# Optimization experiments

Measured on AMD Instinct MI355X. Metric: run time of the kernel, lower is better.

Reference implementation:

```python
import jax, jax.numpy as jnp
import numpy as np

NEG_SLOPE = 0.2   # PyG GATConv default negative_slope
BN_EPS = 1e-5
N_NODES = 50000
N_EDGES = 600000
N_GRAPHS = 64


def _gat_conv(x, W, att_src, att_dst, bias, src, dst, heads, out_ch, concat):
    """PyG GATConv (eval mode, self-loops already appended to src/dst).
    x: [N, in], W: [in, heads*out_ch], att_*: [heads, out_ch], bias: [heads*out_ch] or [out_ch].
    """
    n = x.shape[0]
    h = (x @ W).reshape(n, heads, out_ch)                  # [N, H, C]
    a_s = jnp.sum(h * att_src[None], axis=-1)              # [N, H]
    a_d = jnp.sum(h * att_dst[None], axis=-1)              # [N, H]
    logit = jax.nn.leaky_relu(a_s[src] + a_d[dst], NEG_SLOPE)  # [E, H]
    # segment softmax over destination node (every node has a self-loop -> no empty segment)
    m = jax.ops.segment_max(logit, dst, num_segments=n)
    p = jnp.exp(logit - m[dst])
    denom = jax.ops.segment_sum(p, dst, num_segments=n)
    alpha = p / (denom[dst] + 1e-16)                       # [E, H]
    out = jax.ops.segment_sum(h[src] * alpha[:, :, None], dst, num_segments=n)  # [N, H, C]
    out = out.reshape(n, heads * out_ch) if concat else out.mean(axis=1)
    return out + bias


def _bn(x, gamma, beta):
    mu = x.mean(axis=0)
    var = x.var(axis=0)
    return (x - mu) * jax.lax.rsqrt(var + BN_EPS) * gamma + beta


def setup_inputs() -> dict:
    key = jax.random.key(0)
    ks = jax.random.split(key, 20)
    hidden = 64
    d1_in, d1_out, h1 = 5, hidden // 2, 4          # 5 -> 32x4 = 128
    d2_in, d2_out, h2 = hidden * 2, hidden // 2, 4  # 128 -> 32x4 = 128
    d3_in, d3_out, h3 = hidden * 2, hidden, 1       # 128 -> 64

    def glorot(k, shape):
        fan = shape[0] + shape[-1]
        return jax.random.normal(k, shape, dtype=jnp.float32) * np.sqrt(2.0 / fan)

    inp = {
        "x": jax.random.normal(ks[0], (N_NODES, d1_in), dtype=jnp.float32),
        "edge_index": jax.random.randint(ks[1], (2, N_EDGES), 0, N_NODES),
        "batch": jnp.sort(jax.random.randint(ks[2], (N_NODES,), 0, N_GRAPHS)),
        # conv1
        "W1": glorot(ks[3], (d1_in, h1 * d1_out)),
        "a1_src": glorot(ks[4], (h1, d1_out)),
        "a1_dst": glorot(ks[5], (h1, d1_out)),
        "b1": jnp.zeros((h1 * d1_out,), dtype=jnp.float32),
        "g1": jnp.ones((h1 * d1_out,), dtype=jnp.float32),
        "be1": jnp.zeros((h1 * d1_out,), dtype=jnp.float32),
        # conv2
        "W2": glorot(ks[6], (d2_in, h2 * d2_out)),
        "a2_src": glorot(ks[7], (h2, d2_out)),
        "a2_dst": glorot(ks[8], (h2, d2_out)),
        "b2": jnp.zeros((h2 * d2_out,), dtype=jnp.float32),
        "g2": jnp.ones((h2 * d2_out,), dtype=jnp.float32),
        "be2": jnp.zeros((h2 * d2_out,), dtype=jnp.float32),
        # conv3 (single head, concat=False)
        "W3": glorot(ks[9], (d3_in, h3 * d3_out)),
        "a3_src": glorot(ks[10], (h3, d3_out)),
        "a3_dst": glorot(ks[11], (h3, d3_out)),
        "b3": jnp.zeros((d3_out,), dtype=jnp.float32),
    }
    return inp


def reference(x, edge_index, batch, W1, a1_src, a1_dst, b1, g1, be1,
              W2, a2_src, a2_dst, b2, g2, be2, W3, a3_src, a3_dst, b3):
    n = x.shape[0]
    loops = jnp.arange(n)
    src = jnp.concatenate([edge_index[0], loops])  # PyG add_self_loops=True
    dst = jnp.concatenate([edge_index[1], loops])

    h = jax.nn.elu(_bn(_gat_conv(x, W1, a1_src, a1_dst, b1, src, dst, 4, 32, True), g1, be1))
    h = jax.nn.elu(_bn(_gat_conv(h, W2, a2_src, a2_dst, b2, src, dst, 4, 32, True), g2, be2))
    h = jax.nn.elu(_gat_conv(h, W3, a3_src, a3_dst, b3, src, dst, 1, 64, False))

    counts = jax.ops.segment_sum(jnp.ones((n,), h.dtype), batch, num_segments=N_GRAPHS)
    mean_pool = jax.ops.segment_sum(h, batch, num_segments=N_GRAPHS) / jnp.maximum(counts, 1.0)[:, None]
    max_pool = jax.ops.segment_max(h, batch, num_segments=N_GRAPHS)
    max_pool = jnp.where(counts[:, None] > 0, max_pool, 0.0)
    return jnp.concatenate([mean_pool, max_pool], axis=1)  # [G, 128]
```

## Files before the change

kernel.cpp:

```cpp
#include <hip/hip_runtime.h>
#include <math.h>

#define NEG_SLOPE 0.2f
#define BN_EPS 1e-5f

typedef __attribute__((ext_vector_type(8))) short short8;
typedef __attribute__((ext_vector_type(4))) float f32x4;

__device__ __forceinline__ float lrelu_f(float x){ return x > 0.f ? x : NEG_SLOPE * x; }
__device__ __forceinline__ float elu_f(float x){ return x > 0.f ? x : __expf(x) - 1.f; }

__device__ __forceinline__ unsigned short f2bf(float f){
    unsigned u = __float_as_uint(f);
    return (unsigned short)((u + 0x7fffu + ((u >> 16) & 1u)) >> 16);
}
__device__ __forceinline__ float bf_lo(unsigned v){ return __uint_as_float(v << 16); }
__device__ __forceinline__ float bf_hi(unsigned v){ return __uint_as_float(v & 0xffff0000u); }
__device__ __forceinline__ float bf2f(unsigned short b){ return __uint_as_float((unsigned)b << 16); }

__device__ __forceinline__ unsigned enc_f(float x){
    unsigned b = __float_as_uint(x);
    return (b & 0x80000000u) ? ~b : (b | 0x80000000u);
}
__device__ __forceinline__ float dec_f(unsigned u){
    return __uint_as_float((u & 0x80000000u) ? (u & 0x7FFFFFFFu) : ~u);
}

__global__ void k_prep(const int* __restrict__ ei, int E0, int N, int Bc, int Bg,
                       const int* __restrict__ batch, int G,
                       int* __restrict__ counts, int* __restrict__ gp,
                       const float* __restrict__ W1, const float* __restrict__ a1s,
                       const float* __restrict__ a1d,
                       const float* __restrict__ W2, const float* __restrict__ W3,
                       unsigned short* __restrict__ wt2, unsigned short* __restrict__ wt3,
                       float* __restrict__ u_s, float* __restrict__ u_d){
    int b = blockIdx.x, tid = threadIdx.x;
    if (b < Bc){
        int i = b * 256 + tid, tot = E0 + N;
        if (i < tot){
            int dst = (i < E0) ? ei[E0 + i] : (i - E0);
            atomicAdd(&counts[dst], 1);
        }
    } else if (b < Bc + Bg){
        int i = (b - Bc) * 256 + tid;
        if (i < N){
            int bb = batch[i];
            if (i == 0){ for (int g = 0; g <= bb; ++g) gp[g] = 0; }
            else { int pb = batch[i - 1]; for (int g = pb + 1; g <= bb; ++g) gp[g] = i; }
            if (i == N - 1){ for (int g = bb + 1; g <= G; ++g) gp[g] = N; }
        }
    } else if (b < Bc + Bg + 96){
        int i = (b - Bc - Bg) * 256 + tid;
        if (i < 128 * 128){
            int k = i / 128, c = i % 128;
            wt2[c * 128 + k] = f2bf(W2[i]);
        } else if (i < 128 * 128 + 128 * 64){
            int j = i - 128 * 128;
            int k = j / 64, c = j % 64;
            wt3[c * 128 + k] = f2bf(W3[j]);
        }
    } else {
        if (tid < 40){
            int t2 = tid % 20;
            int k = t2 / 4, hh = t2 % 4;
            const float* att = (tid < 20) ? a1s : a1d;
            float s = 0.f;
            for (int j = 0; j < 32; ++j) s += W1[k * 128 + hh * 32 + j] * att[hh * 32 + j];
            if (tid < 20) u_s[k * 4 + hh] = s; else u_d[k * 4 + hh] = s;
        }
    }
}

__global__ void k_scan_part(const int* __restrict__ counts, int n, int* __restrict__ part){
    __shared__ int sh[256];
    int tid = threadIdx.x;
    int i = blockIdx.x * 256 + tid;
    int v = (i < n) ? counts[i] : 0;
    sh[tid] = v;
    __syncthreads();
    for (int o = 128; o > 0; o >>= 1){
        if (tid < o) sh[tid] += sh[tid + o];
        __syncthreads();
    }
    if (tid == 0) part[blockIdx.x] = sh[0];
}

__global__ void k_scan_write(const int* __restrict__ counts, const int* __restrict__ part,
                             int n, int* __restrict__ row_ptr){
    __shared__ int sh[256], rsh[256];
    __shared__ int offs;
    int tid = threadIdx.x, bid = blockIdx.x;
    int po = 0;
    for (int j = tid; j < bid; j += 256) po += part[j];
    rsh[tid] = po;
    __syncthreads();
    for (int o = 128; o > 0; o >>= 1){
        if (tid < o) rsh[tid] += rsh[tid + o];
        __syncthreads();
    }
    if (tid == 0) offs = rsh[0];
    __syncthreads();
    int i = bid * 256 + tid;
    int v = (i < n) ? counts[i] : 0;
    sh[tid] = v;
    __syncthreads();
    for (int o = 1; o < 256; o <<= 1){
        int t = (tid >= o) ? sh[tid - o] : 0;
        __syncthreads();
        sh[tid] += t;
        __syncthreads();
    }
    if (i < n) row_ptr[i] = offs + sh[tid] - v;
    if (bid == gridDim.x - 1 && tid == 255) row_ptr[n] = offs + sh[255];
}

__global__ void k_scatter(const int* __restrict__ ei, int E0, int N,
                          const int* __restrict__ row_ptr, int* __restrict__ cursor,
                          int* __restrict__ csr_src){
    int i = blockIdx.x * blockDim.x + threadIdx.x;
    int tot = E0 + N;
    if (i >= tot) return;
    int src, dst;
    if (i < E0){ src = ei[i]; dst = ei[E0 + i]; } else { src = dst = i - E0; }
    int pos = atomicAdd(&cursor[dst], 1);
    csr_src[row_ptr[dst] + pos] = src;
}

__launch_bounds__(512)
__global__ void k_agg1(const float* __restrict__ X, const float* __restrict__ W1,
                       const float* __restrict__ u_s, const float* __restrict__ u_d,
                       const int* __restrict__ row_ptr, const int* __restrict__ csr_src,
                       const float* __restrict__ bias, float* __restrict__ out, int N){
    int wid = threadIdx.x >> 6, lane = threadIdx.x & 63;
    long n = (long)blockIdx.x * 8 + wid;
    if (n >= N) return;
    int hh = lane >> 4;
    int c0 = lane * 2;
    float2 wv[5]; float us[5], ud[5];
#pragma unroll
    for (int k = 0; k < 5; ++k){
        wv[k] = *(const float2*)&W1[k * 128 + c0];
        us[k] = u_s[k * 4 + hh];
        ud[k] = u_d[k * 4 + hh];
    }
    float xd[5];
#pragma unroll
    for (int k = 0; k < 5; ++k) xd[k] = X[n * 5 + k];
    float ad = xd[0]*ud[0] + xd[1]*ud[1] + xd[2]*ud[2] + xd[3]*ud[3] + xd[4]*ud[4];
    int beg = row_ptr[n], end = row_ptr[n + 1];
    float accx = 0.f, accy = 0.f, dn = 0.f;
    int e = beg;
    for (; e + 2 <= end; e += 2){
        int s0 = csr_src[e], s1 = csr_src[e + 1];
        float a0[5], a1[5];
#pragma unroll
        for (int k = 0; k < 5; ++k){ a0[k] = X[(long)s0 * 5 + k]; a1[k] = X[(long)s1 * 5 + k]; }
        float as0 = a0[0]*us[0] + a0[1]*us[1] + a0[2]*us[2] + a0[3]*us[3] + a0[4]*us[4];
        float as1 = a1[0]*us[0] + a1[1]*us[1] + a1[2]*us[2] + a1[3]*us[3] + a1[4]*us[4];
        float p0 = __expf(lrelu_f(as0 + ad));
        float p1 = __expf(lrelu_f(as1 + ad));
        float hx0 = a0[0]*wv[0].x + a0[1]*wv[1].x + a0[2]*wv[2].x + a0[3]*wv[3].x + a0[4]*wv[4].x;
        float hy0 = a0[0]*wv[0].y + a0[1]*wv[1].y + a0[2]*wv[2].y + a0[3]*wv[3].y + a0[4]*wv[4].y;
        float hx1 = a1[0]*wv[0].x + a1[1]*wv[1].x + a1[2]*wv[2].x + a1[3]*wv[3].x + a1[4]*wv[4].x;
        float hy1 = a1[0]*wv[0].y + a1[1]*wv[1].y + a1[2]*wv[2].y + a1[3]*wv[3].y + a1[4]*wv[4].y;
        dn += p0 + p1;
        accx += p0 * hx0 + p1 * hx1;
        accy += p0 * hy0 + p1 * hy1;
    }
    if (e < end){
        int s0 = csr_src[e];
        float a0[5];
#pragma unroll
        for (int k = 0; k < 5; ++k) a0[k] = X[(long)s0 * 5 + k];
        float as0 = a0[0]*us[0] + a0[1]*us[1] + a0[2]*us[2] + a0[3]*us[3] + a0[4]*us[4];
        float p0 = __expf(lrelu_f(as0 + ad));
        float hx0 = a0[0]*wv[0].x + a0[1]*wv[1].x + a0[2]*wv[2].x + a0[3]*wv[3].x + a0[4]*wv[4].x;
        float hy0 = a0[0]*wv[0].y + a0[1]*wv[1].y + a0[2]*wv[2].y + a0[3]*wv[3].y + a0[4]*wv[4].y;
        dn += p0; accx += p0 * hx0; accy += p0 * hy0;
    }
    float inv = 1.f / dn;
    float2 o; o.x = accx * inv + bias[c0]; o.y = accy * inv + bias[c0 + 1];
    *(float2*)&out[n * 128 + c0] = o;
}

template<int OUT, int H, bool BN>
__launch_bounds__(256)
__global__ void k_gemm_mfma(const float* __restrict__ X, const unsigned short* __restrict__ Wt,
                            const float* __restrict__ atts, const float* __restrict__ attd,
                            const float* __restrict__ coefs, const float* __restrict__ coefb,
                            unsigned short* __restrict__ h, float* __restrict__ as_,
                            float* __restrict__ ad_, int N){
    constexpr int TM  = 64;
    constexpr int NCT = OUT / 16;
    constexpr int CPH = NCT / H;
    __shared__ unsigned short Xl[TM * 128];
    __shared__ unsigned short Wl[OUT * 128];
    int tid = threadIdx.x;
    long base = (long)blockIdx.x * TM;

    for (int i = tid; i < OUT * 16; i += 256){
        int r = i >> 4, g = i & 15;
        uint4 v = *(const uint4*)&Wt[r * 128 + g * 8];
        int gs = g ^ (r & 7);
        *(uint4*)&Wl[r * 128 + gs * 8] = v;
    }
    for (int i = tid; i < TM * 16; i += 256){
        int r = i >> 4, g = i & 15;
        long node = base + r;
        uint4 o;
        if (node < N){
            const float* xp = &X[node * 128 + g * 8];
            float f[8];
            *(float4*)&f[0] = *(const float4*)xp;
            *(float4*)&f[4] = *(const float4*)(xp + 4);
#pragma unroll
            for (int j = 0; j < 8; ++j){
                float v = f[j];
                if (BN) v = elu_f(fmaf(v, coefs[g * 8 + j], coefb[g * 8 + j]));
                f[j] = v;
            }
            o.x = (unsigned)f2bf(f[0]) | ((unsigned)f2bf(f[1]) << 16);
            o.y = (unsigned)f2bf(f[2]) | ((unsigned)f2bf(f[3]) << 16);
            o.z = (unsigned)f2bf(f[4]) | ((unsigned)f2bf(f[5]) << 16);
            o.w = (unsigned)f2bf(f[6]) | ((unsigned)f2bf(f[7]) << 16);
        } else {
            o.x = o.y = o.z = o.w = 0u;
        }
        int gs = g ^ (r & 7);
        *(uint4*)&Xl[r * 128 + gs * 8] = o;
    }
    __syncthreads();

    int wid = tid >> 6;
    int lane = tid & 63;
    int lr = lane & 15, lk = lane >> 4;

    short8 afrag[4];
    int arow = wid * 16 + lr;
#pragma unroll
    for (int ks = 0; ks < 4; ++ks){
        int g = ks * 4 + lk;
        int gs = g ^ (arow & 7);
        afrag[ks] = *(const short8*)&Xl[arow * 128 + gs * 8];
    }
    f32x4 acc[NCT];
#pragma unroll
    for (int ct = 0; ct < NCT; ++ct) acc[ct] = (f32x4){0.f, 0.f, 0.f, 0.f};
#pragma unroll
    for (int ct = 0; ct < NCT; ++ct){
        int brow = ct * 16 + lr;
#pragma unroll
        for (int ks = 0; ks < 4; ++ks){
            int g = ks * 4 + lk;
            int gs = g ^ (brow & 7);
            short8 bfrag = *(const short8*)&Wl[brow * 128 + gs * 8];
            acc[ct] = __builtin_amdgcn_mfma_f32_16x16x32_bf16(afrag[ks], bfrag, acc[ct], 0, 0, 0);
        }
    }
    float ps[H][4], pd[H][4];
#pragma unroll
    for (int hh = 0; hh < H; ++hh)
#pragma unroll
        for (int j = 0; j < 4; ++j){ ps[hh][j] = 0.f; pd[hh][j] = 0.f; }
#pragma unroll
    for (int ct = 0; ct < NCT; ++ct){
        int col = ct * 16 + lr;
        int hh = ct / CPH;
        float asv = atts[col], adv = attd[col];
#pragma unroll
        for (int j = 0; j < 4; ++j){
            float v = acc[ct][j];
            long node = base + wid * 16 + lk * 4 + j;
            if (node < N) h[node * OUT + col] = f2bf(v);
            ps[hh][j] += v * asv;
            pd[hh][j] += v * adv;
        }
    }
#pragma unroll
    for (int m = 1; m < 16; m <<= 1){
#pragma unroll
        for (int hh = 0; hh < H; ++hh)
#pragma unroll
            for (int j = 0; j < 4; ++j){
                ps[hh][j] += __shfl_xor(ps[hh][j], m);
                pd[hh][j] += __shfl_xor(pd[hh][j], m);
            }
    }
    if (lr == 0){
#pragma unroll
        for (int j = 0; j < 4; ++j){
            long node = base + wid * 16 + lk * 4 + j;
            if (node < N){
#pragma unroll
                for (int hh = 0; hh < H; ++hh){
                    as_[node * H + hh] = ps[hh][j];
                    ad_[node * H + hh] = pd[hh][j];
                }
            }
        }
    }
}

template<int C, int H, int ACT>
__global__ void k_agg(const unsigned short* __restrict__ h, const float* __restrict__ as_,
                      const float* __restrict__ ad_, const int* __restrict__ row_ptr,
                      const int* __restrict__ csr_src, const float* __restrict__ bias,
                      float* __restrict__ out, int N){
    constexpr int CPL = C / 64;
    constexpr int GROUP = C / H;
    int n = blockIdx.x;
    if (n >= N) return;
    int lane = threadIdx.x;
    int hh = (CPL * lane) / GROUP;
    float ad = ad_[n * H + hh];
    int beg = row_ptr[n], end = row_ptr[n + 1];
    float accx = 0.f, accy = 0.f, dn = 0.f;
    const unsigned* h32 = (const unsigned*)h;
    int e = beg;
    for (; e + 2 <= end; e += 2){
        int s0 = csr_src[e], s1 = csr_src[e + 1];
        float a0 = as_[s0 * H + hh], a1 = as_[s1 * H + hh];
        unsigned v0, v1; unsigned short w0, w1;
        if (CPL == 2){ v0 = h32[(long)s0 * 64 + lane]; v1 = h32[(long)s1 * 64 + lane]; }
        else { w0 = h[(long)s0 * 64 + lane]; w1 = h[(long)s1 * 64 + lane]; }
        float p0 = __expf(lrelu_f(a0 + ad));
        float p1 = __expf(lrelu_f(a1 + ad));
        dn += p0 + p1;
        if (CPL == 2){
            accx += p0 * bf_lo(v0) + p1 * bf_lo(v1);
            accy += p0 * bf_hi(v0) + p1 * bf_hi(v1);
        } else {
            accx += p0 * bf2f(w0) + p1 * bf2f(w1);
        }
    }
    if (e < end){
        int s0 = csr_src[e];
        float p0 = __expf(lrelu_f(as_[s0 * H + hh] + ad));
        dn += p0;
        if (CPL == 2){
            unsigned v0 = h32[(long)s0 * 64 + lane];
            accx += p0 * bf_lo(v0); accy += p0 * bf_hi(v0);
        } else {
            accx += p0 * bf2f(h[(long)s0 * 64 + lane]);
        }
    }
    float inv = 1.f / dn;
    if (CPL == 2){
        float vx = accx * inv + bias[2 * lane];
        float vy = accy * inv + bias[2 * lane + 1];
        if (ACT == 1){ vx = elu_f(vx); vy = elu_f(vy); }
        float2 o; o.x = vx; o.y = vy;
        *(float2*)&out[(long)n * C + 2 * lane] = o;
    } else {
        float v = accx * inv + bias[lane];
        if (ACT == 1) v = elu_f(v);
        out[(long)n * C + lane] = v;
    }
}

__launch_bounds__(256)
__global__ void k_bn_part(const float* __restrict__ x, int N,
                          float* __restrict__ ps, float* __restrict__ pq){
    __shared__ float4 lsum[256], lsq[256];
    int tid = threadIdx.x;
    int cq = tid & 31;
    int rg = tid >> 5;
    int rpb = (N + gridDim.x - 1) / gridDim.x;
    int lo = blockIdx.x * rpb;
    int hi = lo + rpb; if (hi > N) hi = N;
    float4 s = {0.f, 0.f, 0.f, 0.f}, q = {0.f, 0.f, 0.f, 0.f};
    int r = lo + rg;
    for (; r + 24 < hi; r += 32){
        float4 v0 = *(const float4*)&x[(long)r * 128 + cq * 4];
        float4 v1 = *(const float4*)&x[(long)(r + 8) * 128 + cq * 4];
        float4 v2 = *(const float4*)&x[(long)(r + 16) * 128 + cq * 4];
        float4 v3 = *(const float4*)&x[(long)(r + 24) * 128 + cq * 4];
        s.x += v0.x + v1.x + v2.x + v3.x;
        s.y += v0.y + v1.y + v2.y + v3.y;
        s.z += v0.z + v1.z + v2.z + v3.z;
        s.w += v0.w + v1.w + v2.w + v3.w;
        q.x += v0.x * v0.x + v1.x * v1.x + v2.x * v2.x + v3.x * v3.x;
        q.y += v0.y * v0.y + v1.y * v1.y + v2.y * v2.y + v3.y * v3.y;
        q.z += v0.z * v0.z + v1.z * v1.z + v2.z * v2.z + v3.z * v3.z;
        q.w += v0.w * v0.w + v1.w * v1.w + v2.w * v2.w + v3.w * v3.w;
    }
    for (; r < hi; r += 8){
        float4 v = *(const float4*)&x[(long)r * 128 + cq * 4];
        s.x += v.x; s.y += v.y; s.z += v.z; s.w += v.w;
        q.x += v.x * v.x; q.y += v.y * v.y; q.z += v.z * v.z; q.w += v.w * v.w;
    }
    lsum[tid] = s; lsq[tid] = q;
    __syncthreads();
    for (int o = 4; o > 0; o >>= 1){
        if (rg < o){
            float4 s2 = lsum[tid + o * 32], q2 = lsq[tid + o * 32];
            s.x += s2.x; s.y += s2.y; s.z += s2.z; s.w += s2.w;
            q.x += q2.x; q.y += q2.y; q.z += q2.z; q.w += q2.w;
            lsum[tid] = s; lsq[tid] = q;
        }
        __syncthreads();
    }
    if (rg == 0){
        *(float4*)&ps[(long)blockIdx.x * 128 + cq * 4] = s;
        *(float4*)&pq[(long)blockIdx.x * 128 + cq * 4] = q;
    }
}

__launch_bounds__(1024)
__global__ void k_bn_fin(const float* __restrict__ ps, const float* __restrict__ pq, int PB,
                         const float* __restrict__ g, const float* __restrict__ be,
                         float invN, float* __restrict__ cs, float* __restrict__ cb){
    __shared__ float sh_s[1024], sh_q[1024];
    int tid = threadIdx.x;
    int c = tid & 127, sl = tid >> 7;
    float s = 0.f, q = 0.f;
    for (int b = sl; b < PB; b += 8){
        s += ps[(long)b * 128 + c];
        q += pq[(long)b * 128 + c];
    }
    sh_s[tid] = s; sh_q[tid] = q;
    __syncthreads();
    for (int o = 4; o > 0; o >>= 1){
        if (sl < o){
            s += sh_s[tid + o * 128]; q += sh_q[tid + o * 128];
            sh_s[tid] = s; sh_q[tid] = q;
        }
        __syncthreads();
    }
    if (sl == 0){
        float mu = s * invN;
        float var = q * invN - mu * mu;
        float sc = g[c] * rsqrtf(var + BN_EPS);
        cs[c] = sc;
        cb[c] = be[c] - mu * sc;
    }
}

__global__ void k_pool_part(const float* __restrict__ x, const int* __restrict__ gp,
                            float* __restrict__ psum, unsigned* __restrict__ pmax){
    constexpr int S = 16;
    __shared__ float ssum[256], smax[256];
    int g = blockIdx.y;
    int split = blockIdx.x;
    int tid = threadIdx.x;
    int c = tid & 63, sub = tid >> 6;
    int beg = gp[g], end = gp[g + 1];
    int len = end - beg;
    int chunk = (len + S - 1) / S;
    int lo = beg + split * chunk;
    int hi = lo + chunk; if (hi > end) hi = end;
    if (lo >= hi) return;
    float s = 0.f, mx = -1e30f;
    for (int i = lo + sub; i < hi; i += 4){
        float v = x[(long)i * 64 + c];
        s += v; mx = fmaxf(mx, v);
    }
    ssum[tid] = s; smax[tid] = mx;
    __syncthreads();
    if (tid < 64){
        for (int k = 1; k < 4; ++k){ s += ssum[tid + 64 * k]; mx = fmaxf(mx, smax[tid + 64 * k]); }
        atomicAdd(&psum[g * 64 + c], s);
        atomicMax(&pmax[g * 64 + c], enc_f(mx));
    }
}

__global__ void k_pool_fin(const float* __restrict__ psum, const unsigned* __restrict__ pmax,
                           const int* __restrict__ gp, float* __restrict__ out){
    int g = blockIdx.x;
    int c = threadIdx.x;
    int cnt = gp[g + 1] - gp[g];
    float mean = (cnt > 0) ? psum[g * 64 + c] / (float)cnt : 0.f;
    float mx   = (cnt > 0) ? dec_f(pmax[g * 64 + c]) : 0.f;
    out[g * 128 + c]      = mean;
    out[g * 128 + 64 + c] = mx;
}

extern "C" void kernel_launch(void* const* d_in, const int* in_sizes, int n_in,
                              void* d_out, int out_size, void* d_ws, size_t ws_size,
                              hipStream_t stream){
    const float* x   = (const float*)d_in[0];
    const int*   ei  = (const int*)d_in[1];
    const int*   bat = (const int*)d_in[2];
    const float* W1  = (const float*)d_in[3];
    const float* a1s = (const float*)d_in[4];
    const float* a1d = (const float*)d_in[5];
    const float* b1  = (const float*)d_in[6];
    const float* g1  = (const float*)d_in[7];
    const float* be1 = (const float*)d_in[8];
    const float* W2  = (const float*)d_in[9];
    const float* a2s = (const float*)d_in[10];
    const float* a2d = (const float*)d_in[11];
    const float* b2  = (const float*)d_in[12];
    const float* g2  = (const float*)d_in[13];
    const float* be2 = (const float*)d_in[14];
    const float* W3  = (const float*)d_in[15];
    const float* a3s = (const float*)d_in[16];
    const float* a3d = (const float*)d_in[17];
    const float* b3  = (const float*)d_in[18];
    float* out = (float*)d_out;

    int N  = in_sizes[2];
    int E0 = in_sizes[1] / 2;
    int E  = E0 + N;
    const int G = 64;
    int P  = (N + 255) / 256;
    const int PB = 512;

    char* ws = (char*)d_ws;
    size_t off = 0;
    auto alloc = [&](size_t bytes) -> char* {
        char* p = ws + off;
        off += (bytes + 255) & ~(size_t)255;
        return p;
    };
    int*      counts  = (int*)alloc((size_t)N * 4);
    int*      cursor  = (int*)alloc((size_t)N * 4);
    float*    psum    = (float*)alloc((size_t)G * 64 * 4);
    unsigned* pmax    = (unsigned*)alloc((size_t)G * 64 * 4);
    size_t zero_bytes = off;
    int*   part    = (int*)alloc(256 * 4);
    int*   row_ptr = (int*)alloc((size_t)(N + 1) * 4);
    int*   csr     = (int*)alloc((size_t)E * 4);
    int*   gp      = (int*)alloc((size_t)(G + 1) * 4);
    float* as_buf  = (float*)alloc((size_t)N * 4 * 4);
    float* ad_buf  = (float*)alloc((size_t)N * 4 * 4);
    float* coefs   = (float*)alloc(128 * 4);
    float* coefb   = (float*)alloc(128 * 4);
    float* u_s     = (float*)alloc(20 * 4);
    float* u_d     = (float*)alloc(20 * 4);
    float* bn_ps   = (float*)alloc((size_t)PB * 128 * 4);
    float* bn_pq   = (float*)alloc((size_t)PB * 128 * 4);
    unsigned short* wt2 = (unsigned short*)alloc(128 * 128 * 2);
    unsigned short* wt3 = (unsigned short*)alloc(64 * 128 * 2);
    unsigned short* hbuf = (unsigned short*)alloc((size_t)N * 128 * 2);
    float* xcur    = (float*)alloc((size_t)N * 128 * 4);

    hipMemsetAsync(ws, 0, zero_bytes, stream);

    int Bc = (E + 255) / 256, Bg = (N + 255) / 256;
    k_prep<<<Bc + Bg + 96 + 1, 256, 0, stream>>>(ei, E0, N, Bc, Bg, bat, G, counts, gp,
                                                 W1, a1s, a1d, W2, W3, wt2, wt3, u_s, u_d);
    k_scan_part<<<P, 256, 0, stream>>>(counts, N, part);
    k_scan_write<<<P, 256, 0, stream>>>(counts, part, N, row_ptr);
    k_scatter<<<(E + 255) / 256, 256, 0, stream>>>(ei, E0, N, row_ptr, cursor, csr);

    k_agg1<<<(N + 7) / 8, 512, 0, stream>>>(x, W1, u_s, u_d, row_ptr, csr, b1, xcur, N);
    k_bn_part<<<PB, 256, 0, stream>>>(xcur, N, bn_ps, bn_pq);
    k_bn_fin<<<1, 1024, 0, stream>>>(bn_ps, bn_pq, PB, g1, be1, 1.f / N, coefs, coefb);

    k_gemm_mfma<128, 4, true><<<(N + 63) / 64, 256, 0, stream>>>(
        xcur, wt2, a2s, a2d, coefs, coefb, hbuf, as_buf, ad_buf, N);
    k_agg<128, 4, 0><<<N, 64, 0, stream>>>(hbuf, as_buf, ad_buf, row_ptr, csr, b2, xcur, N);
    k_bn_part<<<PB, 256, 0, stream>>>(xcur, N, bn_ps, bn_pq);
    k_bn_fin<<<1, 1024, 0, stream>>>(bn_ps, bn_pq, PB, g2, be2, 1.f / N, coefs, coefb);

    k_gemm_mfma<64, 1, true><<<(N + 63) / 64, 256, 0, stream>>>(
        xcur, wt3, a3s, a3d, coefs, coefb, hbuf, as_buf, ad_buf, N);
    k_agg<64, 1, 1><<<N, 64, 0, stream>>>(hbuf, as_buf, ad_buf, row_ptr, csr, b3, xcur, N);

    {
        dim3 grid(16, G);
        k_pool_part<<<grid, 256, 0, stream>>>(xcur, gp, psum, pmax);
        k_pool_fin<<<G, 64, 0, stream>>>(psum, pmax, gp, out);
    }
}
```

Before: 284.1 us.

## Aggregate raw layer-1 features before projecting with W1, splitting edges across lanes

The first GAT layer now computes attention-weighted sums of the 5-dim input features per head and applies W1 once per node afterwards, using the linearity of the projection. Previously every lane recomputed the full 5x2 projection for every edge. Each node now gets 16 lanes (4 heads x 4 edge slices), whose partial sums are combined with shuffles, and W1 is staged in shared memory. This removes redundant per-edge FMAs and redundant gathers across the wave, at the cost of a small cross-lane reduction and different floating-point summation order.

```diff
diff --git a/kernel.cpp b/kernel.cpp
--- a/kernel.cpp
+++ b/kernel.cpp
@@ -126,61 +126,63 @@
     csr_src[row_ptr[dst] + pos] = src;
 }
 
-__launch_bounds__(512)
-__global__ void k_agg1(const float* __restrict__ X, const float* __restrict__ W1,
-                       const float* __restrict__ u_s, const float* __restrict__ u_d,
-                       const int* __restrict__ row_ptr, const int* __restrict__ csr_src,
-                       const float* __restrict__ bias, float* __restrict__ out, int N){
-    int wid = threadIdx.x >> 6, lane = threadIdx.x & 63;
-    long n = (long)blockIdx.x * 8 + wid;
+__launch_bounds__(256)
+__global__ void k_l1(const float* __restrict__ X, const float* __restrict__ W1,
+                     const float* __restrict__ u_s, const float* __restrict__ u_d,
+                     const int* __restrict__ row_ptr, const int* __restrict__ csr_src,
+                     const float* __restrict__ bias, float* __restrict__ out, int N){
+    __shared__ float Wl[5 * 128];
+    int tid = threadIdx.x;
+    for (int i = tid; i < 5 * 128; i += 256) Wl[i] = W1[i];
+    __syncthreads();
+    int grp = tid >> 4, ln = tid & 15;
+    int hh = ln >> 2, sl = ln & 3;
+    long n = (long)blockIdx.x * 16 + grp;
     if (n >= N) return;
-    int hh = lane >> 4;
-    int c0 = lane * 2;
-    float2 wv[5]; float us[5], ud[5];
-#pragma unroll
-    for (int k = 0; k < 5; ++k){
-        wv[k] = *(const float2*)&W1[k * 128 + c0];
-        us[k] = u_s[k * 4 + hh];
-        ud[k] = u_d[k * 4 + hh];
-    }
-    float xd[5];
-#pragma unroll
-    for (int k = 0; k < 5; ++k) xd[k] = X[n * 5 + k];
-    float ad = xd[0]*ud[0] + xd[1]*ud[1] + xd[2]*ud[2] + xd[3]*ud[3] + xd[4]*ud[4];
+    float us[5], ud[5];
+#pragma unroll
+    for (int k = 0; k < 5; ++k){ us[k] = u_s[k * 4 + hh]; ud[k] = u_d[k * 4 + hh]; }
+    float ad = 0.f;
+#pragma unroll
+    for (int k = 0; k < 5; ++k) ad += X[n * 5 + k] * ud[k];
     int beg = row_ptr[n], end = row_ptr[n + 1];
-    float accx = 0.f, accy = 0.f, dn = 0.f;
-    int e = beg;
-    for (; e + 2 <= end; e += 2){
-        int s0 = csr_src[e], s1 = csr_src[e + 1];
-        float a0[5], a1[5];
-#pragma unroll
-        for (int k = 0; k < 5; ++k){ a0[k] = X[(long)s0 * 5 + k]; a1[k] = X[(long)s1 * 5 + k]; }
-        float as0 = a0[0]*us[0] + a0[1]*us[1] + a0[2]*us[2] + a0[3]*us[3] + a0[4]*us[4];
-        float as1 = a1[0]*us[0] + a1[1]*us[1] + a1[2]*us[2] + a1[3]*us[3] + a1[4]*us[4];
-        float p0 = __expf(lrelu_f(as0 + ad));
-        float p1 = __expf(lrelu_f(as1 + ad));
-        float hx0 = a0[0]*wv[0].x + a0[1]*wv[1].x + a0[2]*wv[2].x + a0[3]*wv[3].x + a0[4]*wv[4].x;
-        float hy0 = a0[0]*wv[0].y + a0[1]*wv[1].y + a0[2]*wv[2].y + a0[3]*wv[3].y + a0[4]*wv[4].y;
-        float hx1 = a1[0]*wv[0].x + a1[1]*wv[1].x + a1[2]*wv[2].x + a1[3]*wv[3].x + a1[4]*wv[4].x;
-        float hy1 = a1[0]*wv[0].y + a1[1]*wv[1].y + a1[2]*wv[2].y + a1[3]*wv[3].y + a1[4]*wv[4].y;
-        dn += p0 + p1;
-        accx += p0 * hx0 + p1 * hx1;
-        accy += p0 * hy0 + p1 * hy1;
-    }
-    if (e < end){
-        int s0 = csr_src[e];
-        float a0[5];
-#pragma unroll
-        for (int k = 0; k < 5; ++k) a0[k] = X[(long)s0 * 5 + k];
-        float as0 = a0[0]*us[0] + a0[1]*us[1] + a0[2]*us[2] + a0[3]*us[3] + a0[4]*us[4];
-        float p0 = __expf(lrelu_f(as0 + ad));
-        float hx0 = a0[0]*wv[0].x + a0[1]*wv[1].x + a0[2]*wv[2].x + a0[3]*wv[3].x + a0[4]*wv[4].x;
-        float hy0 = a0[0]*wv[0].y + a0[1]*wv[1].y + a0[2]*wv[2].y + a0[3]*wv[3].y + a0[4]*wv[4].y;
-        dn += p0; accx += p0 * hx0; accy += p0 * hy0;
+    float y0 = 0.f, y1 = 0.f, y2 = 0.f, y3 = 0.f, y4 = 0.f, dn = 0.f;
+    for (int e = beg + sl; e < end; e += 4){
+        long s = csr_src[e];
+        float x0 = X[s * 5 + 0], x1 = X[s * 5 + 1], x2 = X[s * 5 + 2],
+              x3 = X[s * 5 + 3], x4 = X[s * 5 + 4];
+        float as = x0 * us[0] + x1 * us[1] + x2 * us[2] + x3 * us[3] + x4 * us[4];
+        float p = __expf(lrelu_f(as + ad));
+        dn += p;
+        y0 += p * x0; y1 += p * x1; y2 += p * x2; y3 += p * x3; y4 += p * x4;
+    }
+#pragma unroll
+    for (int m = 1; m < 4; m <<= 1){
+        y0 += __shfl_xor(y0, m); y1 += __shfl_xor(y1, m); y2 += __shfl_xor(y2, m);
+        y3 += __shfl_xor(y3, m); y4 += __shfl_xor(y4, m); dn += __shfl_xor(dn, m);
     }
     float inv = 1.f / dn;
-    float2 o; o.x = accx * inv + bias[c0]; o.y = accy * inv + bias[c0 + 1];
-    *(float2*)&out[n * 128 + c0] = o;
+    y0 *= inv; y1 *= inv; y2 *= inv; y3 *= inv; y4 *= inv;
+    int c0 = ln * 8;
+    const float4* Wl4 = (const float4*)Wl;
+    float4 oa, ob;
+    {
+        float4 w0a = Wl4[0 * 32 + ln * 2], w0b = Wl4[0 * 32 + ln * 2 + 1];
+        float4 w1a = Wl4[1 * 32 + ln * 2], w1b = Wl4[1 * 32 + ln * 2 + 1];
+        float4 w2a = Wl4[2 * 32 + ln * 2], w2b = Wl4[2 * 32 + ln * 2 + 1];
+        float4 w3a = Wl4[3 * 32 + ln * 2], w3b = Wl4[3 * 32 + ln * 2 + 1];
+        float4 w4a = Wl4[4 * 32 + ln * 2], w4b = Wl4[4 * 32 + ln * 2 + 1];
+        oa.x = y0*w0a.x + y1*w1a.x + y2*w2a.x + y3*w3a.x + y4*w4a.x + bias[c0 + 0];
+        oa.y = y0*w0a.y + y1*w1a.y + y2*w2a.y + y3*w3a.y + y4*w4a.y + bias[c0 + 1];
+        oa.z = y0*w0a.z + y1*w1a.z + y2*w2a.z + y3*w3a.z + y4*w4a.z + bias[c0 + 2];
+        oa.w = y0*w0a.w + y1*w1a.w + y2*w2a.w + y3*w3a.w + y4*w4a.w + bias[c0 + 3];
+        ob.x = y0*w0b.x + y1*w1b.x + y2*w2b.x + y3*w3b.x + y4*w4b.x + bias[c0 + 4];
+        ob.y = y0*w0b.y + y1*w1b.y + y2*w2b.y + y3*w3b.y + y4*w4b.y + bias[c0 + 5];
+        ob.z = y0*w0b.z + y1*w1b.z + y2*w2b.z + y3*w3b.z + y4*w4b.z + bias[c0 + 6];
+        ob.w = y0*w0b.w + y1*w1b.w + y2*w2b.w + y3*w3b.w + y4*w4b.w + bias[c0 + 7];
+    }
+    *(float4*)&out[n * 128 + c0] = oa;
+    *(float4*)&out[n * 128 + c0 + 4] = ob;
 }
 
 template<int OUT, int H, bool BN>
@@ -544,7 +546,7 @@
     k_scan_write<<<P, 256, 0, stream>>>(counts, part, N, row_ptr);
     k_scatter<<<(E + 255) / 256, 256, 0, stream>>>(ei, E0, N, row_ptr, cursor, csr);
 
-    k_agg1<<<(N + 7) / 8, 512, 0, stream>>>(x, W1, u_s, u_d, row_ptr, csr, b1, xcur, N);
+    k_l1<<<(N + 15) / 16, 256, 0, stream>>>(x, W1, u_s, u_d, row_ptr, csr, b1, xcur, N);
     k_bn_part<<<PB, 256, 0, stream>>>(xcur, N, bn_ps, bn_pq);
     k_bn_fin<<<1, 1024, 0, stream>>>(bn_ps, bn_pq, PB, g1, be1, 1.f / N, coefs, coefb);
 
```

Measured after the change: 242.5 us. -14.7%, faster.
